# Kernel tuning notes

Hardware: AMD Instinct MI355X
Metric: run time of the kernel (lower is better)

## Reference

```python
import jax, jax.numpy as jnp
import numpy as np

MARGIN = 0.3
NORM_EPS = 1e-12  # torch F.normalize default eps


def setup_inputs() -> dict:
    key = jax.random.key(0)
    k1, k2 = jax.random.split(key)
    embeddings = jax.random.normal(k1, (8192, 128), dtype=jnp.float32)
    labels = jax.random.randint(k2, (8192,), 0, 128, dtype=jnp.int64)
    return {"embeddings": embeddings, "labels": labels}


def _triplet_loss(embeddings, labels):
    # L2-normalize rows (torch F.normalize: x / max(||x||, eps))
    norm = jnp.linalg.norm(embeddings, axis=1, keepdims=True)
    e = embeddings / jnp.maximum(norm, NORM_EPS)

    # pairwise squared Euclidean via gram matrix
    dot = e @ e.T                     # [B, B]
    sq = jnp.diagonal(dot)            # [B]
    d2 = jnp.clip(sq[None, :] - 2.0 * dot + sq[:, None], 0.0)
    zmask = (d2 == 0.0).astype(d2.dtype)
    dist = jnp.sqrt(d2 + zmask * 1e-16) * (1.0 - zmask)  # [B, B]

    # hard mining, fully vectorized over rows
    same = labels[:, None] == labels[None, :]
    eye = jnp.eye(labels.shape[0], dtype=bool)
    pos_mask = same & ~eye
    neg_mask = ~same

    dist_ap = jnp.max(jnp.where(pos_mask, dist, -jnp.inf), axis=1)  # hardest positive
    dist_an = jnp.min(jnp.where(neg_mask, dist, jnp.inf), axis=1)   # hardest negative

    valid = pos_mask.any(axis=1) & neg_mask.any(axis=1)
    # MarginRankingLoss(margin)(dist_an, dist_ap, y=1) = mean relu(dist_ap - dist_an + margin)
    per_row = jnp.maximum(dist_ap - dist_an + MARGIN, 0.0)
    n_valid = jnp.maximum(jnp.sum(valid), 1).astype(dist.dtype)
    loss = jnp.sum(jnp.where(valid, per_row, 0.0)) / n_valid
    return jnp.where(valid.any(), loss, jnp.zeros((), dist.dtype))


def reference(embeddings, labels):
    return _triplet_loss(embeddings, labels)
```

## Files before the change

kernel.cpp:

```cpp
#include <hip/hip_runtime.h>
#include <cmath>

#define BN 8192
#define DIM 128
#define MARGIN_F 0.3f
#define NSPLIT 8
#define CPS 1024
#define NT 8
#define NPART (NSPLIT * 2)
#define FBLK 32
#define IMAX 0x7FFFFFFF
#define IMIN 0x80000000

typedef __attribute__((ext_vector_type(4))) int i32x4;

__device__ __forceinline__ int imin3(int a, int b, int c) { return min(a, min(b, c)); }
__device__ __forceinline__ int imax3(int a, int b, int c) { return max(a, max(b, c)); }

__global__ __launch_bounds__(256) void norm_cvt_k(
    const float* __restrict__ emb, float* __restrict__ sqv, unsigned short* __restrict__ EnQ16)
{
  int w = (blockIdx.x * blockDim.x + threadIdx.x) >> 6;
  int lane = threadIdx.x & 63;
  if (w >= BN) return;
  float2 v = *reinterpret_cast<const float2*>(&emb[w * DIM + lane * 2]);
  float s = v.x * v.x + v.y * v.y;
  #pragma unroll
  for (int off = 32; off > 0; off >>= 1) s += __shfl_xor(s, off);
  float iv = 1.0f / fmaxf(sqrtf(s), 1e-12f);
  if (lane == 0) sqv[w] = s * iv * iv;
  int q0 = (int)rintf(127.0f * v.x * iv);
  int q1 = (int)rintf(127.0f * v.y * iv);
  unsigned short us = (unsigned short)((q0 & 255) | ((q1 & 255) << 8));
  int g = lane >> 3;
  EnQ16[(g * BN + w) * 8 + (lane & 7)] = us;
}

__global__ __launch_bounds__(256, 2) void gram_mine_mfma_k(
    const char* __restrict__ EnQ, const int* __restrict__ lab,
    int* __restrict__ ap_part, int* __restrict__ an_part)
{
  __shared__ __align__(16) char Bs[2][16384];

  const int tid = threadIdx.x;
  const int w = tid >> 6, l = tid & 63;
  const int wr = w >> 1, wc = w & 1;
  const int lrow = l & 15, lkg = l >> 4;

  const int rowBase = blockIdx.x * 128 + wr * 64;
  const int panel   = blockIdx.y * CPS;

  i32x4 a[4][2];
  #pragma unroll
  for (int mi = 0; mi < 4; ++mi)
    #pragma unroll
    for (int kk = 0; kk < 2; ++kk)
      a[mi][kk] = *reinterpret_cast<const i32x4*>(
          EnQ + (((size_t)((kk << 2) + lkg) * BN + rowBase + mi * 16 + lrow) << 4));

  int rlv[4][4];
  #pragma unroll
  for (int mi = 0; mi < 4; ++mi) {
    int rb = rowBase + mi * 16 + lkg * 4;
    #pragma unroll
    for (int r = 0; r < 4; ++r) rlv[mi][r] = lab[rb + r] & 255;
  }

  int ap[4][4], an[4][4];
  #pragma unroll
  for (int mi = 0; mi < 4; ++mi)
    #pragma unroll
    for (int r = 0; r < 4; ++r) { ap[mi][r] = IMAX; an[mi][r] = IMIN; }

  const i32x4 zf = {0, 0, 0, 0};

  auto stage = [&](int buf, int colTile) {
    #pragma unroll
    for (int i = 0; i < 4; ++i) {
      int s0 = (w << 8) + (i << 6);
      int s  = s0 + l;
      const char* gp = EnQ + (((size_t)(s >> 7) * BN + colTile + (s & 127)) << 4);
      __builtin_amdgcn_global_load_lds(
          (const __attribute__((address_space(1))) void*)gp,
          (__attribute__((address_space(3))) void*)(&Bs[buf][s0 * 16]),
          16, 0, 0);
    }
  };

  int cur = 0;

  auto halfMFMA = [&](i32x4 (&A)[4][2], int n0) {
    i32x4 b[2];
    #pragma unroll
    for (int n = 0; n < 2; ++n)
      b[n] = *reinterpret_cast<const i32x4*>(
          &Bs[cur][((0 + lkg) * 128 + wc * 64 + (n0 + n) * 16 + lrow) * 16]);
    #pragma unroll
    for (int mi = 0; mi < 4; ++mi)
      #pragma unroll
      for (int n = 0; n < 2; ++n)
        A[mi][n] = __builtin_amdgcn_mfma_i32_16x16x64_i8(a[mi][0], b[n], zf, 0, 0, 0);
    #pragma unroll
    for (int n = 0; n < 2; ++n)
      b[n] = *reinterpret_cast<const i32x4*>(
          &Bs[cur][((4 + lkg) * 128 + wc * 64 + (n0 + n) * 16 + lrow) * 16]);
    #pragma unroll
    for (int mi = 0; mi < 4; ++mi)
      #pragma unroll
      for (int n = 0; n < 2; ++n)
        A[mi][n] = __builtin_amdgcn_mfma_i32_16x16x64_i8(a[mi][1], b[n], A[mi][n], 0, 0, 0);
  };

  auto mineTile = [&](const i32x4 (&A)[4][2], int l0, int l1, int c0, int c1, bool dg) {
    if (!dg) {
      #pragma unroll
      for (int mi = 0; mi < 4; ++mi)
        #pragma unroll
        for (int r = 0; r < 4; ++r) {
          int d0 = A[mi][0][r], d1 = A[mi][1][r];
          bool s0 = (rlv[mi][r] == l0), s1 = (rlv[mi][r] == l1);
          int p0 = s0 ? d0 : IMAX;
          int p1 = s1 ? d1 : IMAX;
          int q0 = s0 ? IMIN : d0;
          int q1 = s1 ? IMIN : d1;
          ap[mi][r] = imin3(ap[mi][r], p0, p1);
          an[mi][r] = imax3(an[mi][r], q0, q1);
        }
    } else {
      #pragma unroll
      for (int mi = 0; mi < 4; ++mi)
        #pragma unroll
        for (int r = 0; r < 4; ++r) {
          int rloc = mi * 16 + lkg * 4 + r;
          int d0 = A[mi][0][r], d1 = A[mi][1][r];
          bool s0 = (rlv[mi][r] == l0), s1 = (rlv[mi][r] == l1);
          bool e0 = (rloc == c0), e1 = (rloc == c1);
          int p0 = (s0 && !e0) ? d0 : IMAX;
          int p1 = (s1 && !e1) ? d1 : IMAX;
          int q0 = s0 ? IMIN : d0;
          int q1 = s1 ? IMIN : d1;
          ap[mi][r] = imin3(ap[mi][r], p0, p1);
          an[mi][r] = imax3(an[mi][r], q0, q1);
        }
    }
  };

  stage(0, panel);
  __syncthreads();

  i32x4 accA[4][2], accB[4][2];
  int clb[4], clbP[4] = {0, 0, 0, 0};
  bool diagP = false;

  #pragma unroll 1
  for (int ct = 0; ct < NT; ++ct) {
    const int colTile = panel + ct * 128;
    const int colBase = colTile + wc * 64;

    if (ct + 1 < NT) stage(cur ^ 1, colTile + 128);

    #pragma unroll
    for (int ni = 0; ni < 4; ++ni) clb[ni] = lab[colBase + ni * 16 + lrow];
    const bool diag = (rowBase == colBase);

    halfMFMA(accA, 0);
    if (ct > 0) mineTile(accB, clbP[2], clbP[3], 32 + lrow, 48 + lrow, diagP);

    halfMFMA(accB, 2);
    mineTile(accA, clb[0], clb[1], 0 + lrow, 16 + lrow, diag);

    __syncthreads();
    #pragma unroll
    for (int ni = 0; ni < 4; ++ni) clbP[ni] = clb[ni];
    diagP = diag;
    cur ^= 1;
  }
  mineTile(accB, clbP[2], clbP[3], 32 + lrow, 48 + lrow, diagP);

  const int part = blockIdx.y * 2 + wc;
  #pragma unroll
  for (int mi = 0; mi < 4; ++mi)
    #pragma unroll
    for (int r = 0; r < 4; ++r) {
      int p = ap[mi][r], n = an[mi][r];
      #pragma unroll
      for (int off = 1; off < 16; off <<= 1) {
        p = min(p, __shfl_xor(p, off));
        n = max(n, __shfl_xor(n, off));
      }
      if (lrow == 0) {
        int rg = rowBase + mi * 16 + lkg * 4 + r;
        ap_part[part * BN + rg] = p;
        an_part[part * BN + rg] = n;
      }
    }
}

__global__ __launch_bounds__(256) void finalize_a_k(
    const int* __restrict__ ap_part, const int* __restrict__ an_part,
    const float* __restrict__ sqv,
    float* __restrict__ blk_sum, float* __restrict__ blk_cnt)
{
  int r = blockIdx.x * 256 + threadIdx.x;
  int apt = IMAX, ant = IMIN;
  #pragma unroll 8
  for (int s = 0; s < NPART; ++s) {
    apt = min(apt, ap_part[s * BN + r]);
    ant = max(ant, an_part[s * BN + r]);
  }
  float sum = 0.f, cnt = 0.f;
  if (apt != IMAX && ant != IMIN) {
    const float sc = 2.0f / (127.0f * 127.0f);
    float rs1 = sqv[r] + 1.0f;
    float dap = sqrtf(fmaxf(fmaf(-sc, (float)apt, rs1), 0.f));
    float dan = sqrtf(fmaxf(fmaf(-sc, (float)ant, rs1), 0.f));
    sum = fmaxf(dap - dan + MARGIN_F, 0.f);
    cnt = 1.f;
  }
  #pragma unroll
  for (int off = 32; off > 0; off >>= 1) {
    sum += __shfl_xor(sum, off);
    cnt += __shfl_xor(cnt, off);
  }
  __shared__ float ssum[4], scnt[4];
  int wv = threadIdx.x >> 6;
  if ((threadIdx.x & 63) == 0) { ssum[wv] = sum; scnt[wv] = cnt; }
  __syncthreads();
  if (threadIdx.x == 0) {
    blk_sum[blockIdx.x] = ssum[0] + ssum[1] + ssum[2] + ssum[3];
    blk_cnt[blockIdx.x] = scnt[0] + scnt[1] + scnt[2] + scnt[3];
  }
}

__global__ __launch_bounds__(64) void finalize_b_k(
    const float* __restrict__ blk_sum, const float* __restrict__ blk_cnt,
    float* __restrict__ out)
{
  int l = threadIdx.x;
  float s = (l < FBLK) ? blk_sum[l] : 0.f;
  float c = (l < FBLK) ? blk_cnt[l] : 0.f;
  #pragma unroll
  for (int off = 32; off > 0; off >>= 1) {
    s += __shfl_xor(s, off);
    c += __shfl_xor(c, off);
  }
  if (l == 0) out[0] = (c > 0.f) ? (s / c) : 0.f;
}

extern "C" void kernel_launch(void* const* d_in, const int* in_sizes, int n_in,
                              void* d_out, int out_size, void* d_ws, size_t ws_size,
                              hipStream_t stream)
{
  const float* emb = (const float*)d_in[0];
  const int*   lab = (const int*)d_in[1];
  float* out = (float*)d_out;
  float* ws  = (float*)d_ws;

  float* sqv     = ws;
  int*   ap_part = (int*)(sqv + BN);
  int*   an_part = ap_part + NPART * BN;
  float* blk_sum = (float*)(an_part + NPART * BN);
  float* blk_cnt = blk_sum + FBLK;
  char*  EnQ     = (char*)(blk_cnt + FBLK);

  norm_cvt_k<<<dim3(BN / 4), 256, 0, stream>>>(emb, sqv, (unsigned short*)EnQ);
  gram_mine_mfma_k<<<dim3(BN / 128, NSPLIT), 256, 0, stream>>>(EnQ, lab, ap_part, an_part);
  finalize_a_k<<<dim3(FBLK), 256, 0, stream>>>(ap_part, an_part, sqv, blk_sum, blk_cnt);
  finalize_b_k<<<dim3(1), 64, 0, stream>>>(blk_sum, blk_cnt, out);
}
```

Measured before the change: 33.46 us.

## Load B fragments directly from global into registers and pack column labels

The LDS double-buffered staging of B tiles and its per-tile __syncthreads are removed. Each wave now loads its B fragments straight from global memory into registers, software-pipelined one half-tile ahead. Column labels are pre-packed four per 32-bit word in the normalization kernel, so each tile needs one load instead of four. This drops LDS traffic and block barriers, but the two wave rows now fetch the same B data separately through cache, and register pressure rises.

```diff
diff --git a/kernel.cpp b/kernel.cpp
--- a/kernel.cpp
+++ b/kernel.cpp
@@ -18,9 +18,18 @@
 __device__ __forceinline__ int imax3(int a, int b, int c) { return max(a, max(b, c)); }
 
 __global__ __launch_bounds__(256) void norm_cvt_k(
-    const float* __restrict__ emb, float* __restrict__ sqv, unsigned short* __restrict__ EnQ16)
-{
-  int w = (blockIdx.x * blockDim.x + threadIdx.x) >> 6;
+    const float* __restrict__ emb, const int* __restrict__ lab,
+    float* __restrict__ sqv, unsigned short* __restrict__ EnQ16,
+    unsigned* __restrict__ LP)
+{
+  int gt = blockIdx.x * blockDim.x + threadIdx.x;
+  if (gt < 2048) {
+    int base = (gt >> 4) * 64 + (gt & 15);
+    LP[gt] = (unsigned)(lab[base] & 255) | ((unsigned)(lab[base + 16] & 255) << 8) |
+             ((unsigned)(lab[base + 32] & 255) << 16) | ((unsigned)(lab[base + 48] & 255) << 24);
+  }
+
+  int w = gt >> 6;
   int lane = threadIdx.x & 63;
   if (w >= BN) return;
   float2 v = *reinterpret_cast<const float2*>(&emb[w * DIM + lane * 2]);
@@ -38,10 +47,9 @@
 
 __global__ __launch_bounds__(256, 2) void gram_mine_mfma_k(
     const char* __restrict__ EnQ, const int* __restrict__ lab,
+    const unsigned* __restrict__ LP,
     int* __restrict__ ap_part, int* __restrict__ an_part)
 {
-  __shared__ __align__(16) char Bs[2][16384];
-
   const int tid = threadIdx.x;
   const int w = tid >> 6, l = tid & 63;
   const int wr = w >> 1, wc = w & 1;
@@ -74,41 +82,28 @@
 
   const i32x4 zf = {0, 0, 0, 0};
 
-  auto stage = [&](int buf, int colTile) {
-    #pragma unroll
-    for (int i = 0; i < 4; ++i) {
-      int s0 = (w << 8) + (i << 6);
-      int s  = s0 + l;
-      const char* gp = EnQ + (((size_t)(s >> 7) * BN + colTile + (s & 127)) << 4);
-      __builtin_amdgcn_global_load_lds(
-          (const __attribute__((address_space(1))) void*)gp,
-          (__attribute__((address_space(3))) void*)(&Bs[buf][s0 * 16]),
-          16, 0, 0);
+  const int colLane = wc * 64 + lrow;
+  const char* bp0 = EnQ + (((size_t)lkg * BN + panel + colLane) << 4);
+  const char* bp1 = bp0 + ((size_t)BN << 6);
+
+  auto loadHalf = [&](i32x4 (&b)[2][2], const char* p0, const char* p1, int n0) {
+    #pragma unroll
+    for (int n = 0; n < 2; ++n) {
+      b[0][n] = *reinterpret_cast<const i32x4*>(p0 + (n0 + n) * 256);
+      b[1][n] = *reinterpret_cast<const i32x4*>(p1 + (n0 + n) * 256);
     }
   };
-
-  int cur = 0;
-
-  auto halfMFMA = [&](i32x4 (&A)[4][2], int n0) {
-    i32x4 b[2];
-    #pragma unroll
-    for (int n = 0; n < 2; ++n)
-      b[n] = *reinterpret_cast<const i32x4*>(
-          &Bs[cur][((0 + lkg) * 128 + wc * 64 + (n0 + n) * 16 + lrow) * 16]);
+  auto mfmaHalf = [&](i32x4 (&A)[4][2], const i32x4 (&b)[2][2]) {
     #pragma unroll
     for (int mi = 0; mi < 4; ++mi)
       #pragma unroll
       for (int n = 0; n < 2; ++n)
-        A[mi][n] = __builtin_amdgcn_mfma_i32_16x16x64_i8(a[mi][0], b[n], zf, 0, 0, 0);
-    #pragma unroll
-    for (int n = 0; n < 2; ++n)
-      b[n] = *reinterpret_cast<const i32x4*>(
-          &Bs[cur][((4 + lkg) * 128 + wc * 64 + (n0 + n) * 16 + lrow) * 16]);
+        A[mi][n] = __builtin_amdgcn_mfma_i32_16x16x64_i8(a[mi][0], b[0][n], zf, 0, 0, 0);
     #pragma unroll
     for (int mi = 0; mi < 4; ++mi)
       #pragma unroll
       for (int n = 0; n < 2; ++n)
-        A[mi][n] = __builtin_amdgcn_mfma_i32_16x16x64_i8(a[mi][1], b[n], A[mi][n], 0, 0, 0);
+        A[mi][n] = __builtin_amdgcn_mfma_i32_16x16x64_i8(a[mi][1], b[1][n], A[mi][n], 0, 0, 0);
   };
 
   auto mineTile = [&](const i32x4 (&A)[4][2], int l0, int l1, int c0, int c1, bool dg) {
@@ -145,37 +140,35 @@
     }
   };
 
-  stage(0, panel);
-  __syncthreads();
-
   i32x4 accA[4][2], accB[4][2];
-  int clb[4], clbP[4] = {0, 0, 0, 0};
+  i32x4 bA[2][2], bB[2][2];
+  int lprev0 = 0, lprev1 = 0;
   bool diagP = false;
+
+  loadHalf(bA, bp0, bp1, 0);
 
   #pragma unroll 1
   for (int ct = 0; ct < NT; ++ct) {
-    const int colTile = panel + ct * 128;
-    const int colBase = colTile + wc * 64;
-
-    if (ct + 1 < NT) stage(cur ^ 1, colTile + 128);
-
-    #pragma unroll
-    for (int ni = 0; ni < 4; ++ni) clb[ni] = lab[colBase + ni * 16 + lrow];
+    const int colBase = panel + ct * 128 + wc * 64;
     const bool diag = (rowBase == colBase);
 
-    halfMFMA(accA, 0);
-    if (ct > 0) mineTile(accB, clbP[2], clbP[3], 32 + lrow, 48 + lrow, diagP);
-
-    halfMFMA(accB, 2);
-    mineTile(accA, clb[0], clb[1], 0 + lrow, 16 + lrow, diag);
-
-    __syncthreads();
-    #pragma unroll
-    for (int ni = 0; ni < 4; ++ni) clbP[ni] = clb[ni];
-    diagP = diag;
-    cur ^= 1;
-  }
-  mineTile(accB, clbP[2], clbP[3], 32 + lrow, 48 + lrow, diagP);
+    const unsigned LPv = LP[(colBase >> 6) * 16 + lrow];
+    const int l0 = (int)(LPv & 255u),         l1 = (int)((LPv >> 8) & 255u);
+    const int l2 = (int)((LPv >> 16) & 255u), l3 = (int)(LPv >> 24);
+
+    loadHalf(bB, bp0, bp1, 2);
+    mfmaHalf(accA, bA);
+    if (ct > 0) mineTile(accB, lprev0, lprev1, 32 + lrow, 48 + lrow, diagP);
+
+    bp0 += 2048; bp1 += 2048;
+    if (ct + 1 < NT) loadHalf(bA, bp0, bp1, 0);
+
+    mfmaHalf(accB, bB);
+    mineTile(accA, l0, l1, 0 + lrow, 16 + lrow, diag);
+
+    lprev0 = l2; lprev1 = l3; diagP = diag;
+  }
+  mineTile(accB, lprev0, lprev1, 32 + lrow, 48 + lrow, diagP);
 
   const int part = blockIdx.y * 2 + wc;
   #pragma unroll
@@ -256,15 +249,16 @@
   float* out = (float*)d_out;
   float* ws  = (float*)d_ws;
 
-  float* sqv     = ws;
-  int*   ap_part = (int*)(sqv + BN);
-  int*   an_part = ap_part + NPART * BN;
-  float* blk_sum = (float*)(an_part + NPART * BN);
-  float* blk_cnt = blk_sum + FBLK;
-  char*  EnQ     = (char*)(blk_cnt + FBLK);
-
-  norm_cvt_k<<<dim3(BN / 4), 256, 0, stream>>>(emb, sqv, (unsigned short*)EnQ);
-  gram_mine_mfma_k<<<dim3(BN / 128, NSPLIT), 256, 0, stream>>>(EnQ, lab, ap_part, an_part);
+  float*    sqv     = ws;
+  int*      ap_part = (int*)(sqv + BN);
+  int*      an_part = ap_part + NPART * BN;
+  float*    blk_sum = (float*)(an_part + NPART * BN);
+  float*    blk_cnt = blk_sum + FBLK;
+  unsigned* LP      = (unsigned*)(blk_cnt + FBLK);
+  char*     EnQ     = (char*)(LP + 2048);
+
+  norm_cvt_k<<<dim3(BN / 4), 256, 0, stream>>>(emb, lab, sqv, (unsigned short*)EnQ, LP);
+  gram_mine_mfma_k<<<dim3(BN / 128, NSPLIT), 256, 0, stream>>>(EnQ, lab, LP, ap_part, an_part);
   finalize_a_k<<<dim3(FBLK), 256, 0, stream>>>(ap_part, an_part, sqv, blk_sum, blk_cnt);
   finalize_b_k<<<dim3(1), 64, 0, stream>>>(blk_sum, blk_cnt, out);
 }
```

New measurement: 33.26 us. Within noise of the previous version (-0.6%).
